# Kernel optimization log

Measured on AMD Instinct MI355X. Metric: run time of the kernel, lower is better.

Reference implementation:

```python
import jax, jax.numpy as jnp
import numpy as np
from jax import lax

ALPHA = 2.0        # elastic_alpha per axis
SMOOTH_NUM = 4
WIN = 5            # box smoothing window
FS = 11            # elastic field size per dim
SIZE_O = (128, 128, 128)


def _rodrigues(rot):
    # rot: (N,3) angle-axis -> (N,3,3) rotation matrix, with Taylor fallback near 0
    eps = 1e-6
    theta2 = jnp.sum(rot * rot, axis=1, keepdims=True)            # (N,1)
    theta = jnp.sqrt(jnp.maximum(theta2, eps))                    # safe sqrt
    w = rot / (theta + eps)
    wx, wy, wz = w[:, 0:1], w[:, 1:2], w[:, 2:3]
    c = jnp.cos(theta)
    s = jnp.sin(theta)
    k = 1.0 - c
    Rn = jnp.concatenate([
        c + wx * wx * k, wx * wy * k - wz * s, wy * s + wx * wz * k,
        wz * s + wx * wy * k, c + wy * wy * k, -wx * s + wy * wz * k,
        -wy * s + wx * wz * k, wx * s + wy * wz * k, c + wz * wz * k,
    ], axis=1).reshape(-1, 3, 3)
    rx, ry, rz = rot[:, 0:1], rot[:, 1:2], rot[:, 2:3]
    one = jnp.ones_like(rx)
    Rt = jnp.concatenate([one, -rz, ry, rz, one, -rx, -ry, rx, one],
                         axis=1).reshape(-1, 3, 3)
    mask = (theta2 > eps)[:, :, None]                             # (N,1,1)
    return jnp.where(mask, Rn, Rt)


def _box_smooth(d):
    # replicate-pad + mean box filter (torch __smooth_3d__)
    p = WIN // 2
    dp = jnp.pad(d, ((0, 0), (0, 0), (p, p), (p, p), (p, p)), mode='edge')
    k = jnp.ones((1, 1, WIN, WIN, WIN), d.dtype) / float(WIN ** 3)
    return lax.conv_general_dilated(dp, k, (1, 1, 1), 'VALID',
                                    dimension_numbers=('NCDHW', 'OIDHW', 'NCDHW'))


def _resize1d(x, axis, out_size):
    # linear interpolation along one axis, align_corners=False (torch interpolate)
    in_size = x.shape[axis]
    src = (jnp.arange(out_size, dtype=x.dtype) + 0.5) * (in_size / out_size) - 0.5
    src = jnp.clip(src, 0.0, in_size - 1.0)
    i0 = jnp.floor(src).astype(jnp.int32)
    i1 = jnp.minimum(i0 + 1, in_size - 1)
    w = (src - i0.astype(x.dtype))
    shape = [1] * x.ndim
    shape[axis] = out_size
    w = w.reshape(shape)
    x0 = jnp.take(x, i0, axis=axis)
    x1 = jnp.take(x, i1, axis=axis)
    return x0 * (1.0 - w) + x1 * w


def _resize3d(d, size):
    d = _resize1d(d, 2, size[0])
    d = _resize1d(d, 3, size[1])
    d = _resize1d(d, 4, size[2])
    return d


def _grid_sample3d(vol, grid):
    # vol: (N,C,D,H,W), grid: (N,D,H,W,3) normalized (x,y,z); trilinear, zeros pad,
    # align_corners=False (torch grid_sample defaults)
    N, C, D, H, W = vol.shape
    x = ((grid[..., 0] + 1.0) * W - 1.0) * 0.5
    y = ((grid[..., 1] + 1.0) * H - 1.0) * 0.5
    z = ((grid[..., 2] + 1.0) * D - 1.0) * 0.5
    x0f, y0f, z0f = jnp.floor(x), jnp.floor(y), jnp.floor(z)
    wx, wy, wz = x - x0f, y - y0f, z - z0f
    x0 = x0f.astype(jnp.int32)
    y0 = y0f.astype(jnp.int32)
    z0 = z0f.astype(jnp.int32)
    b = jnp.arange(N)[:, None, None, None]

    def gather(zi, yi, xi):
        valid = (zi >= 0) & (zi < D) & (yi >= 0) & (yi < H) & (xi >= 0) & (xi < W)
        v = vol[b, :, jnp.clip(zi, 0, D - 1), jnp.clip(yi, 0, H - 1),
                jnp.clip(xi, 0, W - 1)]                           # (N,Do,Ho,Wo,C)
        return v * valid[..., None].astype(vol.dtype)

    out = (gather(z0, y0, x0) * ((1 - wz) * (1 - wy) * (1 - wx))[..., None]
           + gather(z0, y0, x0 + 1) * ((1 - wz) * (1 - wy) * wx)[..., None]
           + gather(z0, y0 + 1, x0) * ((1 - wz) * wy * (1 - wx))[..., None]
           + gather(z0, y0 + 1, x0 + 1) * ((1 - wz) * wy * wx)[..., None]
           + gather(z0 + 1, y0, x0) * (wz * (1 - wy) * (1 - wx))[..., None]
           + gather(z0 + 1, y0, x0 + 1) * (wz * (1 - wy) * wx)[..., None]
           + gather(z0 + 1, y0 + 1, x0) * (wz * wy * (1 - wx))[..., None]
           + gather(z0 + 1, y0 + 1, x0 + 1) * (wz * wy * wx)[..., None])
    return jnp.transpose(out, (0, 4, 1, 2, 3))


def _field(raw, size):
    # raw uniform field -> scaled, smoothed, cropped, resized displacement (D,H,W)
    d = (raw - 0.5) * 2.0 * ALPHA
    for _ in range(SMOOTH_NUM):
        d = _box_smooth(d)
    p = WIN // 2
    d = d[:, :, p:p + FS, p:p + FS, p:p + FS]
    return _resize3d(d, size)[0, 0]


def _forward(vol, rot, scale, shift, dz, dy, dx):
    N, C, D, H, W = vol.shape
    R = _rodrigues(rot)                                  # (N,3,3)
    A = R * scale[:, None, :]                            # scale multiplies columns
    theta = jnp.concatenate([A, shift[:, :, None]], axis=2)  # (N,3,4)
    # base affine grid, align_corners=False: coord_i = (2i+1)/S - 1
    xs = (2.0 * jnp.arange(W, dtype=vol.dtype) + 1.0) / W - 1.0
    ys = (2.0 * jnp.arange(H, dtype=vol.dtype) + 1.0) / H - 1.0
    zs = (2.0 * jnp.arange(D, dtype=vol.dtype) + 1.0) / D - 1.0
    zz, yy, xx = jnp.meshgrid(zs, ys, xs, indexing='ij')
    pts = jnp.stack([xx, yy, zz, jnp.ones_like(xx)], axis=-1)    # (D,H,W,4)
    grid = jnp.einsum('nij,dhwj->ndhwi', theta, pts)             # (N,D,H,W,3)
    disp = jnp.stack([_field(dz, (D, H, W)), _field(dy, (D, H, W)),
                      _field(dx, (D, H, W))], axis=-1)           # (D,H,W,3)
    grid = grid + disp[None]
    out = _grid_sample3d(vol, grid)
    # central crop to SIZE_O
    zs0 = D // 2 - SIZE_O[0] // 2
    ys0 = H // 2 - SIZE_O[1] // 2
    xs0 = W // 2 - SIZE_O[2] // 2
    return out[:, :, zs0:zs0 + SIZE_O[0], ys0:ys0 + SIZE_O[1], xs0:xs0 + SIZE_O[2]]


def setup_inputs() -> dict:
    key = jax.random.key(0)
    k = jax.random.split(key, 7)
    vol = jax.random.normal(k[0], (4, 1, 160, 160, 160), dtype=jnp.float32)
    rot = (jax.random.uniform(k[1], (4, 3), dtype=jnp.float32) - 0.5) * 0.35   # ~±10 deg in rad
    scale = 0.9 + 0.2 * jax.random.uniform(k[2], (4, 3), dtype=jnp.float32)
    shift = (jax.random.uniform(k[3], (4, 3), dtype=jnp.float32) - 0.5) * 0.1
    dz = jax.random.uniform(k[4], (1, 1, 15, 15, 15), dtype=jnp.float32)
    dy = jax.random.uniform(k[5], (1, 1, 15, 15, 15), dtype=jnp.float32)
    dx = jax.random.uniform(k[6], (1, 1, 15, 15, 15), dtype=jnp.float32)
    return {"vol": vol, "rot": rot, "scale": scale, "shift": shift,
            "dz": dz, "dy": dy, "dx": dx}


def reference(vol, rot, scale, shift, dz, dy, dx):
    return _forward(vol, rot, scale, shift, dz, dy, dx)
```

## Files before the change

kernel.cpp:

```cpp
#include <hip/hip_runtime.h>

#define VD 160
#define OD 128
#define CROP0 16
#define FSZ 11
#define RAWSZ 15
#define NBATCH 4
#define ODQ 4

#define ESTR 17
#define EOH  (8*ESTR)
#define ECH  (8*8*ESTR)

struct M15 { float v[15][15]; };
constexpr M15 mkB() {
    M15 b{};
    for (int i = 0; i < 15; ++i)
        for (int j = 0; j < 15; ++j) b.v[i][j] = 0.0f;
    for (int i = 0; i < 15; ++i)
        for (int t = -2; t <= 2; ++t) {
            int j = i + t; j = j < 0 ? 0 : (j > 14 ? 14 : j);
            b.v[i][j] += 0.2f;
        }
    return b;
}
constexpr M15 mmul(const M15& a, const M15& b) {
    M15 c{};
    for (int i = 0; i < 15; ++i)
        for (int j = 0; j < 15; ++j) {
            float s = 0.0f;
            for (int k = 0; k < 15; ++k) s += a.v[i][k] * b.v[k][j];
            c.v[i][j] = s;
        }
    return c;
}
constexpr M15 B2 = mmul(mkB(), mkB());
constexpr M15 B4 = mmul(B2, B2);

__global__ __launch_bounds__(1024) void prep_kernel(
        const float* __restrict__ rot, const float* __restrict__ scale,
        const float* __restrict__ shift,
        const float* __restrict__ dz, const float* __restrict__ dy,
        const float* __restrict__ dx,
        float* __restrict__ theta, float* __restrict__ fields) {
    const int tid = threadIdx.x;
    const int chan = blockIdx.x;

    if (chan == 3) {
        int n = tid;
        if (n >= NBATCH) return;
        float rx = rot[n*3+0], ry = rot[n*3+1], rz = rot[n*3+2];
        float t2 = rx*rx + ry*ry + rz*rz;
        const float eps = 1e-6f;
        float th = sqrtf(fmaxf(t2, eps));
        float inv = 1.0f / (th + eps);
        float wx = rx*inv, wy = ry*inv, wz = rz*inv;
        float c = cosf(th), s = sinf(th), k = 1.0f - c;
        float R[9];
        if (t2 > eps) {
            R[0] = c + wx*wx*k;      R[1] = wx*wy*k - wz*s;  R[2] = wy*s + wx*wz*k;
            R[3] = wz*s + wx*wy*k;   R[4] = c + wy*wy*k;     R[5] = -wx*s + wy*wz*k;
            R[6] = -wy*s + wx*wz*k;  R[7] = wx*s + wy*wz*k;  R[8] = c + wz*wz*k;
        } else {
            R[0] = 1.0f; R[1] = -rz;  R[2] = ry;
            R[3] = rz;   R[4] = 1.0f; R[5] = -rx;
            R[6] = -ry;  R[7] = rx;   R[8] = 1.0f;
        }
        for (int i = 0; i < 3; ++i) {
            for (int j = 0; j < 3; ++j)
                theta[n*12 + i*4 + j] = R[i*3 + j] * scale[n*3 + j];
            theta[n*12 + i*4 + 3] = shift[n*3 + i];
        }
        return;
    }

    __shared__ float bufA[RAWSZ*RAWSZ*RAWSZ];
    __shared__ float bufB[RAWSZ*RAWSZ*FSZ];
    __shared__ float bufC[RAWSZ*FSZ*FSZ];
    const float* raw = (chan == 0) ? dz : (chan == 1) ? dy : dx;
    const int NTOT = RAWSZ*RAWSZ*RAWSZ;

    for (int i = tid; i < NTOT; i += 1024)
        bufA[i] = (raw[i] - 0.5f) * 4.0f;
    __syncthreads();

    for (int i = tid; i < RAWSZ*RAWSZ*FSZ; i += 1024) {
        const int zy = i / FSZ;
        const int xo = i % FSZ;
        const float* row = &bufA[zy * RAWSZ];
        const float* w = B4.v[xo + 2];
        float s = 0.0f;
        #pragma unroll
        for (int j = 0; j < RAWSZ; ++j) s += row[j] * w[j];
        bufB[i] = s;
    }
    __syncthreads();

    for (int i = tid; i < RAWSZ*FSZ*FSZ; i += 1024) {
        const int z  = i / (FSZ*FSZ);
        const int r  = i % (FSZ*FSZ);
        const int yo = r / FSZ;
        const int xo = r % FSZ;
        const float* base = &bufB[z * (RAWSZ*FSZ) + xo];
        const float* w = B4.v[yo + 2];
        float s = 0.0f;
        #pragma unroll
        for (int j = 0; j < RAWSZ; ++j) s += base[j * FSZ] * w[j];
        bufC[i] = s;
    }
    __syncthreads();

    for (int i = tid; i < FSZ*FSZ*FSZ; i += 1024) {
        const int zo = i / (FSZ*FSZ);
        const int r  = i % (FSZ*FSZ);
        const float* base = &bufC[r];
        const float* w = B4.v[zo + 2];
        float s = 0.0f;
        #pragma unroll
        for (int j = 0; j < RAWSZ; ++j) s += base[j * (FSZ*FSZ)] * w[j];
        fields[chan*FSZ*FSZ*FSZ + i] = s;
    }
}

__device__ __forceinline__ void resize_coord(int m, int& i0, int& i1, float& w) {
    float s = fmaf((float)m + 0.5f, (float)FSZ / (float)VD, -0.5f);
    s = fminf(fmaxf(s, 0.0f), (float)(FSZ - 1));
    float f = floorf(s);
    i0 = (int)f;
    i1 = min(i0 + 1, FSZ - 1);
    w = s - f;
}

__global__ __launch_bounds__(512, 4) void sample_kernel(
        const float* __restrict__ vol, const float* __restrict__ theta,
        const float* __restrict__ fields, float* __restrict__ out) {
    __shared__ float e[3*ECH];

    const int tid  = threadIdx.x;
    const int lane = tid & 63;
    const int wl   = lane & 15;
    const int hl   = lane >> 4;
    const int wv   = tid >> 6;
    const int wx   = wv & 1;
    const int wh   = (wv >> 1) & 1;
    const int wd   = wv >> 2;

    const int ow_l = (wx << 4) | wl;
    const int oh_l = (wh << 2) | hl;
    const int ow   = (blockIdx.x << 5) | ow_l;
    const int oh   = (blockIdx.y << 3) | oh_l;
    const int odb  = (blockIdx.z & 15) << 3;
    const int n    = blockIdx.z >> 4;

    {
        const int xi   = tid & 15;
        const int row0 = tid >> 4;
        if (xi < FSZ) {
            const int eod  = row0 & 7;
            const int eoh0 = row0 >> 3;
            int zi0, zi1, yA0, yA1, yB0, yB1;
            float zw, ywA, ywB;
            resize_coord(odb + eod + CROP0, zi0, zi1, zw);
            const int hbase = (blockIdx.y << 3) + CROP0;
            resize_coord(hbase + eoh0,     yA0, yA1, ywA);
            resize_coord(hbase + eoh0 + 4, yB0, yB1, ywB);
            const float wz0 = 1.0f - zw;
            const float wA00 = wz0*(1.0f-ywA), wA01 = wz0*ywA;
            const float wA10 = zw*(1.0f-ywA),  wA11 = zw*ywA;
            const float wB00 = wz0*(1.0f-ywB), wB01 = wz0*ywB;
            const float wB10 = zw*(1.0f-ywB),  wB11 = zw*ywB;
            const int oA00 = zi0*121 + yA0*11 + xi, oA01 = zi0*121 + yA1*11 + xi;
            const int oA10 = zi1*121 + yA0*11 + xi, oA11 = zi1*121 + yA1*11 + xi;
            const int oB00 = zi0*121 + yB0*11 + xi, oB01 = zi0*121 + yB1*11 + xi;
            const int oB10 = zi1*121 + yB0*11 + xi, oB11 = zi1*121 + yB1*11 + xi;
            float* ew = &e[row0*ESTR + xi];
            #pragma unroll
            for (int i = 0; i < 6; ++i) {
                const float* f = fields + (i >> 1) * (FSZ*FSZ*FSZ);
                float v;
                if (i & 1)
                    v = f[oB00]*wB00 + f[oB01]*wB01 + f[oB10]*wB10 + f[oB11]*wB11;
                else
                    v = f[oA00]*wA00 + f[oA01]*wA01 + f[oA10]*wA10 + f[oA11]*wA11;
                ew[i * (32*ESTR)] = v * 80.0f;
            }
        }
    }

    const int w_ = ow + CROP0;
    const int h_ = oh + CROP0;

    const float x = fmaf(2.0f * (float)w_ + 1.0f, 1.0f / (float)VD, -1.0f);
    const float y = fmaf(2.0f * (float)h_ + 1.0f, 1.0f / (float)VD, -1.0f);

    float s = fmaf((float)w_ + 0.5f, (float)FSZ / (float)VD, -0.5f);
    s = fminf(fmaxf(s, 0.0f), (float)(FSZ - 1));
    const float sf = floorf(s);
    const int   xi0 = (int)sf;
    const float xw  = s - sf;

    const float* th = theta + n*12;
    const float cx = fmaf(th[0]*x + th[1]*y + th[3], 80.0f, 79.5f);
    const float cy = fmaf(th[4]*x + th[5]*y + th[7], 80.0f, 79.5f);
    const float cz = fmaf(th[8]*x + th[9]*y + th[11], 80.0f, 79.5f);
    const float tz0 = th[2] * 80.0f, tz1 = th[6] * 80.0f, tz2 = th[10] * 80.0f;

    const float* v = vol + (size_t)n * (VD*VD*VD);

    const float* ebase = &e[oh_l*EOH + (wd << 2)*ESTR + xi0];

    const int dbase = odb + (wd << 2) + CROP0;
    const float zb = fmaf(2.0f * (float)dbase + 1.0f, 1.0f / (float)VD, -1.0f);
    float* op = out + ((((size_t)n*OD + (odb + (wd << 2)))*OD + oh)*OD + ow);

    __syncthreads();

    float ex0[ODQ], ex1[ODQ], ey0[ODQ], ey1[ODQ], ez0[ODQ], ez1[ODQ];
    #pragma unroll
    for (int k = 0; k < ODQ; ++k) {
        ex0[k] = ebase[        k*ESTR    ];  ex1[k] = ebase[        k*ESTR + 1];
        ey0[k] = ebase[ECH   + k*ESTR    ];  ey1[k] = ebase[ECH   + k*ESTR + 1];
        ez0[k] = ebase[2*ECH + k*ESTR    ];  ez1[k] = ebase[2*ECH + k*ESTR + 1];
    }

    float fx[ODQ], fy[ODQ], fz[ODQ];
    int ix[ODQ], iy[ODQ], iz[ODQ];
    int inb = 1;
    #pragma unroll
    for (int k = 0; k < ODQ; ++k) {
        const float z = zb + (float)k * (2.0f / (float)VD);
        const float d80x = fmaf(ex1[k] - ex0[k], xw, ex0[k]);
        const float d80y = fmaf(ey1[k] - ey0[k], xw, ey0[k]);
        const float d80z = fmaf(ez1[k] - ez0[k], xw, ez0[k]);
        const float xs = fmaf(tz0, z, cx) + d80x;
        const float ys = fmaf(tz1, z, cy) + d80y;
        const float zs = fmaf(tz2, z, cz) + d80z;
        const float x0f = floorf(xs), y0f = floorf(ys), z0f = floorf(zs);
        fx[k] = xs - x0f; fy[k] = ys - y0f; fz[k] = zs - z0f;
        ix[k] = (int)x0f; iy[k] = (int)y0f; iz[k] = (int)z0f;
        inb &= ((unsigned)ix[k] < (unsigned)(VD-1)) &
               ((unsigned)iy[k] < (unsigned)(VD-1)) &
               ((unsigned)iz[k] < (unsigned)(VD-1));
    }

    if (__all(inb)) {
        float2 p00[ODQ], p01[ODQ], p10[ODQ], p11[ODQ];
        #pragma unroll
        for (int k = 0; k < ODQ; ++k) {
            const int b00 = (iz[k]*VD + iy[k])*VD + ix[k];
            __builtin_memcpy(&p00[k], v + b00,            sizeof(float2));
            __builtin_memcpy(&p01[k], v + b00 + VD,       sizeof(float2));
            __builtin_memcpy(&p10[k], v + b00 + VD*VD,    sizeof(float2));
            __builtin_memcpy(&p11[k], v + b00 + VD*VD+VD, sizeof(float2));
        }
        #pragma unroll
        for (int k = 0; k < ODQ; ++k) {
            const float r00 = fmaf(fx[k], p00[k].y - p00[k].x, p00[k].x);
            const float r01 = fmaf(fx[k], p01[k].y - p01[k].x, p01[k].x);
            const float r10 = fmaf(fx[k], p10[k].y - p10[k].x, p10[k].x);
            const float r11 = fmaf(fx[k], p11[k].y - p11[k].x, p11[k].x);
            const float r0 = fmaf(fy[k], r01 - r00, r00);
            const float r1 = fmaf(fy[k], r11 - r10, r10);
            const float r  = fmaf(fz[k], r1 - r0, r0);
            __builtin_nontemporal_store(r, op + (size_t)k*OD*OD);
        }
    } else {
        #pragma unroll
        for (int k = 0; k < ODQ; ++k) {
            const int ix1 = ix[k] + 1, iy1 = iy[k] + 1, iz1 = iz[k] + 1;

            const float WX0 = ((unsigned)ix[k] < (unsigned)VD) ? (1.0f - fx[k]) : 0.0f;
            const float WX1 = ((unsigned)ix1   < (unsigned)VD) ? fx[k]          : 0.0f;
            const float WY0 = ((unsigned)iy[k] < (unsigned)VD) ? (1.0f - fy[k]) : 0.0f;
            const float WY1 = ((unsigned)iy1   < (unsigned)VD) ? fy[k]          : 0.0f;
            const float WZ0 = ((unsigned)iz[k] < (unsigned)VD) ? (1.0f - fz[k]) : 0.0f;
            const float WZ1 = ((unsigned)iz1   < (unsigned)VD) ? fz[k]          : 0.0f;

            const int xc0 = min(max(ix[k], 0), VD-1), xc1 = min(max(ix1, 0), VD-1);
            const int yc0 = min(max(iy[k], 0), VD-1), yc1 = min(max(iy1, 0), VD-1);
            const int zc0 = min(max(iz[k], 0), VD-1), zc1 = min(max(iz1, 0), VD-1);

            const int base = min(xc0, VD-2);
            const bool hi0 = (xc0 != base);
            const bool hi1 = (xc1 != base);
            const float wA = (hi0 ? 0.0f : WX0) + (hi1 ? 0.0f : WX1);
            const float wB = (hi0 ? WX0 : 0.0f) + (hi1 ? WX1 : 0.0f);

            const int sA = zc0*(VD*VD), sB = zc1*(VD*VD);
            const int tA = yc0*VD + base, tB = yc1*VD + base;

            float2 p00, p01, p10, p11;
            __builtin_memcpy(&p00, v + sA + tA, sizeof(float2));
            __builtin_memcpy(&p01, v + sA + tB, sizeof(float2));
            __builtin_memcpy(&p10, v + sB + tA, sizeof(float2));
            __builtin_memcpy(&p11, v + sB + tB, sizeof(float2));

            const float r00 = p00.x*wA + p00.y*wB;
            const float r01 = p01.x*wA + p01.y*wB;
            const float r10 = p10.x*wA + p10.y*wB;
            const float r11 = p11.x*wA + p11.y*wB;
            const float r = (r00*WY0 + r01*WY1)*WZ0 + (r10*WY0 + r11*WY1)*WZ1;

            __builtin_nontemporal_store(r, op + (size_t)k*OD*OD);
        }
    }
}

extern "C" void kernel_launch(void* const* d_in, const int* in_sizes, int n_in,
                              void* d_out, int out_size, void* d_ws, size_t ws_size,
                              hipStream_t stream) {
    const float* vol   = (const float*)d_in[0];
    const float* rot   = (const float*)d_in[1];
    const float* scale = (const float*)d_in[2];
    const float* shift = (const float*)d_in[3];
    const float* dz    = (const float*)d_in[4];
    const float* dy    = (const float*)d_in[5];
    const float* dx    = (const float*)d_in[6];
    float* out = (float*)d_out;

    float* ws     = (float*)d_ws;
    float* theta  = ws;
    float* fields = ws + 48;

    prep_kernel<<<4, 1024, 0, stream>>>(rot, scale, shift, dz, dy, dx,
                                        theta, fields);
    dim3 grid(OD/32, OD/8, (OD/8)*NBATCH);
    sample_kernel<<<grid, 512, 0, stream>>>(vol, theta, fields, out);
}
```

Before: 143.6 us.

## Precompute z/y-resized displacement table in separate kernel, drop shared memory stage

Adds an etab_kernel that precomputes the displacement field, resized along z and y for every (od, oh) row and scaled by 80, into a global table padded to 16 per row. The sampler then reads its six displacement values straight from global memory instead of building a shared-memory tile and calling __syncthreads. This removes per-block redundant interpolation and the barrier, at the cost of an extra launch and about 3 MB of global table traffic. It also adds sched_barrier hints to keep loads grouped, and replaces nontemporal output stores with plain stores.

```diff
diff --git a/kernel.cpp b/kernel.cpp
--- a/kernel.cpp
+++ b/kernel.cpp
@@ -8,9 +8,9 @@
 #define NBATCH 4
 #define ODQ 4
 
-#define ESTR 17
-#define EOH  (8*ESTR)
-#define ECH  (8*8*ESTR)
+#define EPAD 16
+#define E_K  (OD*EPAD)
+#define E_C  (OD*OD*EPAD)
 
 struct M15 { float v[15][15]; };
 constexpr M15 mkB() {
@@ -131,11 +131,38 @@
     w = s - f;
 }
 
+__global__ __launch_bounds__(128) void etab_kernel(
+        const float* __restrict__ fields, float* __restrict__ etab) {
+    const int od = blockIdx.x;
+    const int oh = threadIdx.x;
+    int zi0, zi1, yi0, yi1; float zw, yw;
+    resize_coord(od + CROP0, zi0, zi1, zw);
+    resize_coord(oh + CROP0, yi0, yi1, yw);
+    const float w00 = (1.0f-zw)*(1.0f-yw), w01 = (1.0f-zw)*yw;
+    const float w10 = zw*(1.0f-yw),        w11 = zw*yw;
+    #pragma unroll
+    for (int c = 0; c < 3; ++c) {
+        const float* f = fields + c * (FSZ*FSZ*FSZ);
+        const float* r00 = f + zi0*121 + yi0*11;
+        const float* r01 = f + zi0*121 + yi1*11;
+        const float* r10 = f + zi1*121 + yi0*11;
+        const float* r11 = f + zi1*121 + yi1*11;
+        float vv[EPAD];
+        #pragma unroll
+        for (int xi = 0; xi < FSZ; ++xi)
+            vv[xi] = 80.0f * (r00[xi]*w00 + r01[xi]*w01 + r10[xi]*w10 + r11[xi]*w11);
+        #pragma unroll
+        for (int xi = FSZ; xi < EPAD; ++xi) vv[xi] = 0.0f;
+        float4* dst = (float4*)(etab + ((size_t)c*OD + od)*E_K + (size_t)oh*EPAD);
+        #pragma unroll
+        for (int q = 0; q < EPAD/4; ++q)
+            dst[q] = make_float4(vv[4*q], vv[4*q+1], vv[4*q+2], vv[4*q+3]);
+    }
+}
+
 __global__ __launch_bounds__(512, 4) void sample_kernel(
         const float* __restrict__ vol, const float* __restrict__ theta,
-        const float* __restrict__ fields, float* __restrict__ out) {
-    __shared__ float e[3*ECH];
-
+        const float* __restrict__ etab, float* __restrict__ out) {
     const int tid  = threadIdx.x;
     const int lane = tid & 63;
     const int wl   = lane & 15;
@@ -145,53 +172,16 @@
     const int wh   = (wv >> 1) & 1;
     const int wd   = wv >> 2;
 
-    const int ow_l = (wx << 4) | wl;
-    const int oh_l = (wh << 2) | hl;
-    const int ow   = (blockIdx.x << 5) | ow_l;
-    const int oh   = (blockIdx.y << 3) | oh_l;
+    const int ow   = (blockIdx.x << 5) | (wx << 4) | wl;
+    const int oh   = (blockIdx.y << 3) | (wh << 2) | hl;
     const int odb  = (blockIdx.z & 15) << 3;
     const int n    = blockIdx.z >> 4;
-
-    {
-        const int xi   = tid & 15;
-        const int row0 = tid >> 4;
-        if (xi < FSZ) {
-            const int eod  = row0 & 7;
-            const int eoh0 = row0 >> 3;
-            int zi0, zi1, yA0, yA1, yB0, yB1;
-            float zw, ywA, ywB;
-            resize_coord(odb + eod + CROP0, zi0, zi1, zw);
-            const int hbase = (blockIdx.y << 3) + CROP0;
-            resize_coord(hbase + eoh0,     yA0, yA1, ywA);
-            resize_coord(hbase + eoh0 + 4, yB0, yB1, ywB);
-            const float wz0 = 1.0f - zw;
-            const float wA00 = wz0*(1.0f-ywA), wA01 = wz0*ywA;
-            const float wA10 = zw*(1.0f-ywA),  wA11 = zw*ywA;
-            const float wB00 = wz0*(1.0f-ywB), wB01 = wz0*ywB;
-            const float wB10 = zw*(1.0f-ywB),  wB11 = zw*ywB;
-            const int oA00 = zi0*121 + yA0*11 + xi, oA01 = zi0*121 + yA1*11 + xi;
-            const int oA10 = zi1*121 + yA0*11 + xi, oA11 = zi1*121 + yA1*11 + xi;
-            const int oB00 = zi0*121 + yB0*11 + xi, oB01 = zi0*121 + yB1*11 + xi;
-            const int oB10 = zi1*121 + yB0*11 + xi, oB11 = zi1*121 + yB1*11 + xi;
-            float* ew = &e[row0*ESTR + xi];
-            #pragma unroll
-            for (int i = 0; i < 6; ++i) {
-                const float* f = fields + (i >> 1) * (FSZ*FSZ*FSZ);
-                float v;
-                if (i & 1)
-                    v = f[oB00]*wB00 + f[oB01]*wB01 + f[oB10]*wB10 + f[oB11]*wB11;
-                else
-                    v = f[oA00]*wA00 + f[oA01]*wA01 + f[oA10]*wA10 + f[oA11]*wA11;
-                ew[i * (32*ESTR)] = v * 80.0f;
-            }
-        }
-    }
+    const int od0  = odb + (wd << 2);
 
     const int w_ = ow + CROP0;
-    const int h_ = oh + CROP0;
 
     const float x = fmaf(2.0f * (float)w_ + 1.0f, 1.0f / (float)VD, -1.0f);
-    const float y = fmaf(2.0f * (float)h_ + 1.0f, 1.0f / (float)VD, -1.0f);
+    const float y = fmaf(2.0f * (float)(oh + CROP0) + 1.0f, 1.0f / (float)VD, -1.0f);
 
     float s = fmaf((float)w_ + 0.5f, (float)FSZ / (float)VD, -0.5f);
     s = fminf(fmaxf(s, 0.0f), (float)(FSZ - 1));
@@ -207,31 +197,28 @@
 
     const float* v = vol + (size_t)n * (VD*VD*VD);
 
-    const float* ebase = &e[oh_l*EOH + (wd << 2)*ESTR + xi0];
-
-    const int dbase = odb + (wd << 2) + CROP0;
-    const float zb = fmaf(2.0f * (float)dbase + 1.0f, 1.0f / (float)VD, -1.0f);
-    float* op = out + ((((size_t)n*OD + (odb + (wd << 2)))*OD + oh)*OD + ow);
-
-    __syncthreads();
-
-    float ex0[ODQ], ex1[ODQ], ey0[ODQ], ey1[ODQ], ez0[ODQ], ez1[ODQ];
+    const float* ep = etab + (size_t)od0*E_K + (size_t)oh*EPAD + xi0;
+    float e0[3][ODQ], e1[3][ODQ];
     #pragma unroll
-    for (int k = 0; k < ODQ; ++k) {
-        ex0[k] = ebase[        k*ESTR    ];  ex1[k] = ebase[        k*ESTR + 1];
-        ey0[k] = ebase[ECH   + k*ESTR    ];  ey1[k] = ebase[ECH   + k*ESTR + 1];
-        ez0[k] = ebase[2*ECH + k*ESTR    ];  ez1[k] = ebase[2*ECH + k*ESTR + 1];
-    }
-
+    for (int c = 0; c < 3; ++c)
+        #pragma unroll
+        for (int k = 0; k < ODQ; ++k) {
+            e0[c][k] = ep[c*E_C + k*E_K    ];
+            e1[c][k] = ep[c*E_C + k*E_K + 1];
+        }
+    __builtin_amdgcn_sched_barrier(0);
+
+    const float zb = fmaf(2.0f * (float)(od0 + CROP0) + 1.0f,
+                          1.0f / (float)VD, -1.0f);
     float fx[ODQ], fy[ODQ], fz[ODQ];
     int ix[ODQ], iy[ODQ], iz[ODQ];
     int inb = 1;
     #pragma unroll
     for (int k = 0; k < ODQ; ++k) {
         const float z = zb + (float)k * (2.0f / (float)VD);
-        const float d80x = fmaf(ex1[k] - ex0[k], xw, ex0[k]);
-        const float d80y = fmaf(ey1[k] - ey0[k], xw, ey0[k]);
-        const float d80z = fmaf(ez1[k] - ez0[k], xw, ez0[k]);
+        const float d80x = fmaf(e1[0][k] - e0[0][k], xw, e0[0][k]);
+        const float d80y = fmaf(e1[1][k] - e0[1][k], xw, e0[1][k]);
+        const float d80z = fmaf(e1[2][k] - e0[2][k], xw, e0[2][k]);
         const float xs = fmaf(tz0, z, cx) + d80x;
         const float ys = fmaf(tz1, z, cy) + d80y;
         const float zs = fmaf(tz2, z, cz) + d80z;
@@ -243,6 +230,8 @@
                ((unsigned)iz[k] < (unsigned)(VD-1));
     }
 
+    float* op = out + ((((size_t)n*OD + od0)*OD + oh)*OD + ow);
+
     if (__all(inb)) {
         float2 p00[ODQ], p01[ODQ], p10[ODQ], p11[ODQ];
         #pragma unroll
@@ -253,6 +242,7 @@
             __builtin_memcpy(&p10[k], v + b00 + VD*VD,    sizeof(float2));
             __builtin_memcpy(&p11[k], v + b00 + VD*VD+VD, sizeof(float2));
         }
+        __builtin_amdgcn_sched_barrier(0);
         #pragma unroll
         for (int k = 0; k < ODQ; ++k) {
             const float r00 = fmaf(fx[k], p00[k].y - p00[k].x, p00[k].x);
@@ -261,8 +251,7 @@
             const float r11 = fmaf(fx[k], p11[k].y - p11[k].x, p11[k].x);
             const float r0 = fmaf(fy[k], r01 - r00, r00);
             const float r1 = fmaf(fy[k], r11 - r10, r10);
-            const float r  = fmaf(fz[k], r1 - r0, r0);
-            __builtin_nontemporal_store(r, op + (size_t)k*OD*OD);
+            op[(size_t)k*OD*OD] = fmaf(fz[k], r1 - r0, r0);
         }
     } else {
         #pragma unroll
@@ -299,9 +288,7 @@
             const float r01 = p01.x*wA + p01.y*wB;
             const float r10 = p10.x*wA + p10.y*wB;
             const float r11 = p11.x*wA + p11.y*wB;
-            const float r = (r00*WY0 + r01*WY1)*WZ0 + (r10*WY0 + r11*WY1)*WZ1;
-
-            __builtin_nontemporal_store(r, op + (size_t)k*OD*OD);
+            op[(size_t)k*OD*OD] = (r00*WY0 + r01*WY1)*WZ0 + (r10*WY0 + r11*WY1)*WZ1;
         }
     }
 }
@@ -321,9 +308,11 @@
     float* ws     = (float*)d_ws;
     float* theta  = ws;
     float* fields = ws + 48;
+    float* etab   = ws + 4096;
 
     prep_kernel<<<4, 1024, 0, stream>>>(rot, scale, shift, dz, dy, dx,
                                         theta, fields);
+    etab_kernel<<<OD, 128, 0, stream>>>(fields, etab);
     dim3 grid(OD/32, OD/8, (OD/8)*NBATCH);
-    sample_kernel<<<grid, 512, 0, stream>>>(vol, theta, fields, out);
-}
+    sample_kernel<<<grid, 512, 0, stream>>>(vol, theta, etab, out);
+}
```

After: 148.7 us. 1.04x slower.
